# Kernel optimization log

Measured on AMD Instinct MI355X. Metric: run time of the kernel, lower is better.

Reference implementation:

```python
import jax, jax.numpy as jnp
import numpy as np

EPS = 1e-05


def setup_inputs() -> dict:
    key = jax.random.key(0)
    ks = jax.random.split(key, 4)
    B, N, D, H, E = 16, 8192, 128, 64, 64
    x = jax.random.normal(ks[0], (B, N, D), dtype=jnp.float32)
    ln_w = jnp.ones((D,), jnp.float32)
    ln_b = jnp.zeros((D,), jnp.float32)
    Wl = jax.random.normal(ks[1], (D, H), dtype=jnp.float32) / np.sqrt(D)
    bl = jnp.zeros((H,), jnp.float32)
    Wr = jax.random.normal(ks[2], (D, H), dtype=jnp.float32) / np.sqrt(D)
    br = jnp.zeros((H,), jnp.float32)
    Wo = jax.random.normal(ks[3], (H, E), dtype=jnp.float32) / np.sqrt(H)
    bo = jnp.zeros((E,), jnp.float32)
    return {"x": x, "ln_w": ln_w, "ln_b": ln_b, "Wl": Wl, "bl": bl,
            "Wr": Wr, "br": br, "Wo": Wo, "bo": bo}


def _layernorm(x, w, b):
    mu = jnp.mean(x, axis=-1, keepdims=True)
    var = jnp.mean(jnp.square(x - mu), axis=-1, keepdims=True)
    return (x - mu) * jax.lax.rsqrt(var + EPS) * w + b


def reference(x, ln_w, ln_b, Wl, bl, Wr, br, Wo, bo):
    # x: [B, N, D]
    xn = _layernorm(x, ln_w, ln_b)
    left = xn @ Wl + bl    # [B, N, H]
    right = xn @ Wr + br   # [B, N, H]
    # Original: einsum('b i d, b j d -> b i j d').mean(dim=1).
    # Identical math without the O(N^2) tensor: mean over i factors out of
    # the product since left[b,i,d]*right[b,j,d] is separable in i.
    outer = left.mean(axis=1)[:, None, :] * right  # [B, N, H]
    return outer @ Wo + bo  # [B, N, E]
```

## Files before the change

kernel.cpp:

```cpp
#include <hip/hip_runtime.h>
#include <math.h>

#define B_  16
#define N_  8192
#define D_  128
#define H_  64
#define E_  64
#define EPSLN 1e-5f

typedef __attribute__((ext_vector_type(8))) short short8;
typedef __attribute__((ext_vector_type(4))) float f32x4;

#define WSB_COL 0
#define WSB_MT  8192
#define WSB_T   270336
#define WSB_C   274432

static __device__ __forceinline__ unsigned short f2bf(float f) {
    union { float f; unsigned u; } c; c.f = f;
    unsigned u = c.u;
    return (unsigned short)((u + 0x7FFFu + ((u >> 16) & 1u)) >> 16);
}

__global__ __launch_bounds__(256) void k_stats(const float* __restrict__ x,
                                               float* __restrict__ colacc) {
    __shared__ float xs[64 * 132];
    __shared__ float mul[64], rsl[64], red[128];
    int b = blockIdx.y, t = threadIdx.x;
    int rowbase = blockIdx.x * 64;
    size_t gbase = (size_t)(b * N_ + rowbase) * 32;

    const float4* x4 = (const float4*)x;
#pragma unroll
    for (int k = 0; k < 8; ++k) {
        int idx = t + 256 * k;
        int row = idx >> 5, c4 = idx & 31;
        *(float4*)&xs[row * 132 + c4 * 4] = x4[gbase + idx];
    }
    __syncthreads();

    {
        int r = t >> 2, q = t & 3;
        float s = 0.f, s2 = 0.f;
#pragma unroll
        for (int i = 0; i < 8; ++i) {
            float4 v = *(const float4*)&xs[r * 132 + q * 32 + i * 4];
            s  += (v.x + v.y) + (v.z + v.w);
            s2 += (v.x * v.x + v.y * v.y) + (v.z * v.z + v.w * v.w);
        }
        s  += __shfl_xor(s, 1, 64);  s  += __shfl_xor(s, 2, 64);
        s2 += __shfl_xor(s2, 1, 64); s2 += __shfl_xor(s2, 2, 64);
        if (q == 0) {
            float mu  = s * (1.f / D_);
            float var = s2 * (1.f / D_) - mu * mu;
            mul[r] = mu;
            rsl[r] = rsqrtf(var + EPSLN);
        }
    }
    __syncthreads();

    int c = t & 127, hh = t >> 7;
    float acc = 0.f;
#pragma unroll 8
    for (int i = 0; i < 32; ++i) {
        int r = hh * 32 + i;
        acc += rsl[r] * (xs[r * 132 + c] - mul[r]);
    }
    if (hh == 1) red[c] = acc;
    __syncthreads();
    if (hh == 0) atomicAdd(&colacc[b * D_ + c], acc + red[c]);
}

__global__ __launch_bounds__(256) void k_combine(const float* __restrict__ colacc,
                                                 const float* __restrict__ ln_w,
                                                 const float* __restrict__ ln_b,
                                                 const float* __restrict__ Wl,
                                                 const float* __restrict__ bl,
                                                 const float* __restrict__ Wr,
                                                 const float* __restrict__ br,
                                                 const float* __restrict__ Wo,
                                                 const float* __restrict__ bo,
                                                 unsigned short* __restrict__ Mt,
                                                 float* __restrict__ Tg,
                                                 float* __restrict__ Cg) {
    int b = blockIdx.y, dblk = blockIdx.x, t = threadIdx.x;
    __shared__ float cm[D_], ml[H_], uu[H_], qq[H_];
    __shared__ float P[H_ * E_];

    if (t < D_) cm[t] = ln_w[t] * colacc[b * D_ + t] * (1.f / N_) + ln_b[t];
    __syncthreads();

    if (t < H_) {
        float a = bl[t], u = 0.f, q = 0.f;
        for (int d = 0; d < D_; ++d) {
            float wr = Wr[d * H_ + t];
            a += cm[d] * Wl[d * H_ + t];
            u += ln_w[d] * wr;
            q += ln_b[d] * wr;
        }
        ml[t] = a; uu[t] = u; qq[t] = q + br[t];
    }
    __syncthreads();

#pragma unroll
    for (int k = 0; k < 16; ++k) {
        int idx = t + 256 * k;
        P[idx] = ml[idx >> 6] * Wo[idx];
    }
    __syncthreads();

    int d  = dblk * 32 + (t >> 3);
    int eo = (t & 7) * 8;
    float a0 = 0, a1 = 0, a2 = 0, a3 = 0, a4 = 0, a5 = 0, a6 = 0, a7 = 0;
    for (int h = 0; h < H_; ++h) {
        float wr = Wr[d * H_ + h];
        const float4* p4 = (const float4*)&P[h * E_ + eo];
        float4 pa = p4[0], pb = p4[1];
        a0 += wr * pa.x; a1 += wr * pa.y; a2 += wr * pa.z; a3 += wr * pa.w;
        a4 += wr * pb.x; a5 += wr * pb.y; a6 += wr * pb.z; a7 += wr * pb.w;
    }
    float wd = ln_w[d];
    size_t mb = (size_t)b * E_ * D_;
    Mt[mb + (size_t)(eo + 0) * D_ + d] = f2bf(wd * a0);
    Mt[mb + (size_t)(eo + 1) * D_ + d] = f2bf(wd * a1);
    Mt[mb + (size_t)(eo + 2) * D_ + d] = f2bf(wd * a2);
    Mt[mb + (size_t)(eo + 3) * D_ + d] = f2bf(wd * a3);
    Mt[mb + (size_t)(eo + 4) * D_ + d] = f2bf(wd * a4);
    Mt[mb + (size_t)(eo + 5) * D_ + d] = f2bf(wd * a5);
    Mt[mb + (size_t)(eo + 6) * D_ + d] = f2bf(wd * a6);
    Mt[mb + (size_t)(eo + 7) * D_ + d] = f2bf(wd * a7);

    if (dblk == 0 && t < E_) {
        float T = 0.f, C = bo[t];
        for (int h = 0; h < H_; ++h) {
            float p = P[h * E_ + t];
            T += uu[h] * p;
            C += qq[h] * p;
        }
        Tg[b * E_ + t] = T;
        Cg[b * E_ + t] = C;
    }
}

__global__ __launch_bounds__(256, 2) void k_gemm(const float* __restrict__ x,
                                                 const unsigned short* __restrict__ Mt,
                                                 const float* __restrict__ Tg,
                                                 const float* __restrict__ Cg,
                                                 float* __restrict__ out) {
    __shared__ short xs[256 * 128];
    __shared__ float mul[256], rsl[256], Tl[E_], Cl[E_];

    int b = blockIdx.y, t = threadIdx.x;
    int rowbase = blockIdx.x * 256;

    if (t < E_) { Tl[t] = Tg[b * E_ + t]; Cl[t] = Cg[b * E_ + t]; }

    {
        const float4* xrow = (const float4*)(x + (size_t)(b * N_ + rowbase + t) * D_);
        float s = 0.f, s2 = 0.f;
        int sw = t & 15;
#pragma unroll
        for (int g = 0; g < 16; ++g) {
            float4 va = xrow[2 * g], vb = xrow[2 * g + 1];
            s  += (va.x + va.y) + (va.z + va.w) + (vb.x + vb.y) + (vb.z + vb.w);
            s2 += (va.x * va.x + va.y * va.y) + (va.z * va.z + va.w * va.w)
                + (vb.x * vb.x + vb.y * vb.y) + (vb.z * vb.z + vb.w * vb.w);
            short8 sv;
            sv[0] = (short)f2bf(va.x); sv[1] = (short)f2bf(va.y);
            sv[2] = (short)f2bf(va.z); sv[3] = (short)f2bf(va.w);
            sv[4] = (short)f2bf(vb.x); sv[5] = (short)f2bf(vb.y);
            sv[6] = (short)f2bf(vb.z); sv[7] = (short)f2bf(vb.w);
            *(short8*)&xs[t * 128 + ((g ^ sw) * 8)] = sv;
        }
        float mu  = s * (1.f / D_);
        float var = s2 * (1.f / D_) - mu * mu;
        mul[t] = mu;
        rsl[t] = rsqrtf(var + EPSLN);
    }
    __syncthreads();

    int wv = t >> 6, lane = t & 63;
    int m16 = lane & 15, quad = lane >> 4;

    f32x4 acc[4][4];
#pragma unroll
    for (int i = 0; i < 4; ++i)
#pragma unroll
        for (int j = 0; j < 4; ++j) acc[i][j] = (f32x4){0.f, 0.f, 0.f, 0.f};

    const unsigned short* Mb = Mt + (size_t)b * E_ * D_;

#pragma unroll
    for (int kc = 0; kc < 4; ++kc) {
        short8 af[4], bf[4];
#pragma unroll
        for (int mt = 0; mt < 4; ++mt) {
            int row = wv * 64 + mt * 16 + m16;
            int g = kc * 4 + quad;
            af[mt] = *(const short8*)&xs[row * 128 + ((g ^ m16) * 8)];
        }
#pragma unroll
        for (int nt = 0; nt < 4; ++nt) {
            bf[nt] = *(const short8*)(Mb + (size_t)(nt * 16 + m16) * D_ + kc * 32 + quad * 8);
        }
#pragma unroll
        for (int mt = 0; mt < 4; ++mt)
#pragma unroll
            for (int nt = 0; nt < 4; ++nt)
                acc[mt][nt] = __builtin_amdgcn_mfma_f32_16x16x32_bf16(
                    af[mt], bf[nt], acc[mt][nt], 0, 0, 0);
    }

    size_t outbase = (size_t)(b * N_ + rowbase) * E_;
#pragma unroll
    for (int mt = 0; mt < 4; ++mt) {
        int rb = wv * 64 + mt * 16 + quad * 4;
        float mu0 = mul[rb + 0], rs0 = rsl[rb + 0];
        float mu1 = mul[rb + 1], rs1 = rsl[rb + 1];
        float mu2 = mul[rb + 2], rs2 = rsl[rb + 2];
        float mu3 = mul[rb + 3], rs3 = rsl[rb + 3];
#pragma unroll
        for (int nt = 0; nt < 4; ++nt) {
            int col = nt * 16 + m16;
            float Tc = Tl[col], Cc = Cl[col];
            float* o = out + outbase + (size_t)rb * E_ + col;
            o[0 * E_] = rs0 * (acc[mt][nt][0] - mu0 * Tc) + Cc;
            o[1 * E_] = rs1 * (acc[mt][nt][1] - mu1 * Tc) + Cc;
            o[2 * E_] = rs2 * (acc[mt][nt][2] - mu2 * Tc) + Cc;
            o[3 * E_] = rs3 * (acc[mt][nt][3] - mu3 * Tc) + Cc;
        }
    }
}

extern "C" void kernel_launch(void* const* d_in, const int* in_sizes, int n_in,
                              void* d_out, int out_size, void* d_ws, size_t ws_size,
                              hipStream_t stream) {
    const float* x    = (const float*)d_in[0];
    const float* ln_w = (const float*)d_in[1];
    const float* ln_b = (const float*)d_in[2];
    const float* Wl   = (const float*)d_in[3];
    const float* bl   = (const float*)d_in[4];
    const float* Wr   = (const float*)d_in[5];
    const float* br   = (const float*)d_in[6];
    const float* Wo   = (const float*)d_in[7];
    const float* bo   = (const float*)d_in[8];
    float* out = (float*)d_out;
    char* ws   = (char*)d_ws;

    float*          colacc = (float*)(ws + WSB_COL);
    unsigned short* Mt     = (unsigned short*)(ws + WSB_MT);
    float*          Tg     = (float*)(ws + WSB_T);
    float*          Cg     = (float*)(ws + WSB_C);

    hipMemsetAsync(colacc, 0, B_ * D_ * sizeof(float), stream);

    k_stats<<<dim3(N_ / 64, B_), 256, 0, stream>>>(x, colacc);
    k_combine<<<dim3(4, B_), 256, 0, stream>>>(colacc, ln_w, ln_b, Wl, bl, Wr,
                                               br, Wo, bo, Mt, Tg, Cg);
    k_gemm<<<dim3(N_ / 256, B_), 256, 0, stream>>>(x, Mt, Tg, Cg, out);
}
```

Baseline: 145.1 us.

## Reassociate outer-product GEMM to read x once via bf16 right intermediate

Drops the separate stats pass over x. The first GEMM pass now computes right = LN(x)@Wr in bf16, writes it to a workspace buffer, and in the same pass produces per-block column partial sums of normalized x. A small combine kernel then builds the per-batch left-mean-scaled Wo matrix and bias. A second MFMA pass multiplies right by that matrix to form the output. This removes one full 64 MB read of x at the cost of writing and re-reading a 16 MB bf16 intermediate, an extra launch, and column sums taken from bf16-rounded x.

```diff
diff --git a/kernel.cpp b/kernel.cpp
--- a/kernel.cpp
+++ b/kernel.cpp
@@ -11,149 +11,66 @@
 typedef __attribute__((ext_vector_type(8))) short short8;
 typedef __attribute__((ext_vector_type(4))) float f32x4;
 
-#define WSB_COL 0
-#define WSB_MT  8192
-#define WSB_T   270336
-#define WSB_C   274432
+#define WSB_PART 0
+#define WSB_WRT  262144
+#define WSB_U    278528
+#define WSB_Q    278784
+#define WSB_W2T  279040
+#define WSB_C2   410112
+#define WSB_Z    1048576
 
 static __device__ __forceinline__ unsigned short f2bf(float f) {
     union { float f; unsigned u; } c; c.f = f;
     unsigned u = c.u;
     return (unsigned short)((u + 0x7FFFu + ((u >> 16) & 1u)) >> 16);
 }
-
-__global__ __launch_bounds__(256) void k_stats(const float* __restrict__ x,
-                                               float* __restrict__ colacc) {
-    __shared__ float xs[64 * 132];
-    __shared__ float mul[64], rsl[64], red[128];
-    int b = blockIdx.y, t = threadIdx.x;
-    int rowbase = blockIdx.x * 64;
-    size_t gbase = (size_t)(b * N_ + rowbase) * 32;
-
-    const float4* x4 = (const float4*)x;
-#pragma unroll
-    for (int k = 0; k < 8; ++k) {
-        int idx = t + 256 * k;
-        int row = idx >> 5, c4 = idx & 31;
-        *(float4*)&xs[row * 132 + c4 * 4] = x4[gbase + idx];
-    }
-    __syncthreads();
-
-    {
-        int r = t >> 2, q = t & 3;
-        float s = 0.f, s2 = 0.f;
-#pragma unroll
-        for (int i = 0; i < 8; ++i) {
-            float4 v = *(const float4*)&xs[r * 132 + q * 32 + i * 4];
-            s  += (v.x + v.y) + (v.z + v.w);
-            s2 += (v.x * v.x + v.y * v.y) + (v.z * v.z + v.w * v.w);
-        }
-        s  += __shfl_xor(s, 1, 64);  s  += __shfl_xor(s, 2, 64);
-        s2 += __shfl_xor(s2, 1, 64); s2 += __shfl_xor(s2, 2, 64);
-        if (q == 0) {
-            float mu  = s * (1.f / D_);
-            float var = s2 * (1.f / D_) - mu * mu;
-            mul[r] = mu;
-            rsl[r] = rsqrtf(var + EPSLN);
-        }
-    }
-    __syncthreads();
-
-    int c = t & 127, hh = t >> 7;
-    float acc = 0.f;
-#pragma unroll 8
+static __device__ __forceinline__ float bf2f(short v) {
+    union { unsigned u; float f; } c;
+    c.u = ((unsigned)(unsigned short)v) << 16;
+    return c.f;
+}
+
+__global__ __launch_bounds__(256) void k_prep(const float* __restrict__ ln_w,
+                                              const float* __restrict__ ln_b,
+                                              const float* __restrict__ Wr,
+                                              unsigned short* __restrict__ Wrt,
+                                              float* __restrict__ ug,
+                                              float* __restrict__ qg) {
+    __shared__ float ru[4][H_], rq[4][H_];
+    int t = threadIdx.x;
+    int h = t & 63, dq = t >> 6;
+    float u = 0.f, q = 0.f;
     for (int i = 0; i < 32; ++i) {
-        int r = hh * 32 + i;
-        acc += rsl[r] * (xs[r * 132 + c] - mul[r]);
-    }
-    if (hh == 1) red[c] = acc;
-    __syncthreads();
-    if (hh == 0) atomicAdd(&colacc[b * D_ + c], acc + red[c]);
-}
-
-__global__ __launch_bounds__(256) void k_combine(const float* __restrict__ colacc,
-                                                 const float* __restrict__ ln_w,
-                                                 const float* __restrict__ ln_b,
-                                                 const float* __restrict__ Wl,
-                                                 const float* __restrict__ bl,
-                                                 const float* __restrict__ Wr,
-                                                 const float* __restrict__ br,
-                                                 const float* __restrict__ Wo,
-                                                 const float* __restrict__ bo,
-                                                 unsigned short* __restrict__ Mt,
-                                                 float* __restrict__ Tg,
-                                                 float* __restrict__ Cg) {
-    int b = blockIdx.y, dblk = blockIdx.x, t = threadIdx.x;
-    __shared__ float cm[D_], ml[H_], uu[H_], qq[H_];
-    __shared__ float P[H_ * E_];
-
-    if (t < D_) cm[t] = ln_w[t] * colacc[b * D_ + t] * (1.f / N_) + ln_b[t];
-    __syncthreads();
-
+        int d = dq * 32 + i;
+        float wr = Wr[d * H_ + h];
+        float lw = ln_w[d];
+        u += lw * wr;
+        q += ln_b[d] * wr;
+        Wrt[h * D_ + d] = f2bf(lw * wr);
+    }
+    ru[dq][h] = u; rq[dq][h] = q;
+    __syncthreads();
     if (t < H_) {
-        float a = bl[t], u = 0.f, q = 0.f;
-        for (int d = 0; d < D_; ++d) {
-            float wr = Wr[d * H_ + t];
-            a += cm[d] * Wl[d * H_ + t];
-            u += ln_w[d] * wr;
-            q += ln_b[d] * wr;
-        }
-        ml[t] = a; uu[t] = u; qq[t] = q + br[t];
-    }
-    __syncthreads();
-
-#pragma unroll
-    for (int k = 0; k < 16; ++k) {
-        int idx = t + 256 * k;
-        P[idx] = ml[idx >> 6] * Wo[idx];
-    }
-    __syncthreads();
-
-    int d  = dblk * 32 + (t >> 3);
-    int eo = (t & 7) * 8;
-    float a0 = 0, a1 = 0, a2 = 0, a3 = 0, a4 = 0, a5 = 0, a6 = 0, a7 = 0;
-    for (int h = 0; h < H_; ++h) {
-        float wr = Wr[d * H_ + h];
-        const float4* p4 = (const float4*)&P[h * E_ + eo];
-        float4 pa = p4[0], pb = p4[1];
-        a0 += wr * pa.x; a1 += wr * pa.y; a2 += wr * pa.z; a3 += wr * pa.w;
-        a4 += wr * pb.x; a5 += wr * pb.y; a6 += wr * pb.z; a7 += wr * pb.w;
-    }
-    float wd = ln_w[d];
-    size_t mb = (size_t)b * E_ * D_;
-    Mt[mb + (size_t)(eo + 0) * D_ + d] = f2bf(wd * a0);
-    Mt[mb + (size_t)(eo + 1) * D_ + d] = f2bf(wd * a1);
-    Mt[mb + (size_t)(eo + 2) * D_ + d] = f2bf(wd * a2);
-    Mt[mb + (size_t)(eo + 3) * D_ + d] = f2bf(wd * a3);
-    Mt[mb + (size_t)(eo + 4) * D_ + d] = f2bf(wd * a4);
-    Mt[mb + (size_t)(eo + 5) * D_ + d] = f2bf(wd * a5);
-    Mt[mb + (size_t)(eo + 6) * D_ + d] = f2bf(wd * a6);
-    Mt[mb + (size_t)(eo + 7) * D_ + d] = f2bf(wd * a7);
-
-    if (dblk == 0 && t < E_) {
-        float T = 0.f, C = bo[t];
-        for (int h = 0; h < H_; ++h) {
-            float p = P[h * E_ + t];
-            T += uu[h] * p;
-            C += qq[h] * p;
-        }
-        Tg[b * E_ + t] = T;
-        Cg[b * E_ + t] = C;
-    }
-}
-
-__global__ __launch_bounds__(256, 2) void k_gemm(const float* __restrict__ x,
-                                                 const unsigned short* __restrict__ Mt,
-                                                 const float* __restrict__ Tg,
-                                                 const float* __restrict__ Cg,
-                                                 float* __restrict__ out) {
+        ug[t] = ru[0][t] + ru[1][t] + ru[2][t] + ru[3][t];
+        qg[t] = rq[0][t] + rq[1][t] + rq[2][t] + rq[3][t];
+    }
+}
+
+__global__ __launch_bounds__(256, 2) void k_pass1(const float* __restrict__ x,
+                                                  const unsigned short* __restrict__ Wrt,
+                                                  const float* __restrict__ ug,
+                                                  const float* __restrict__ qg,
+                                                  float* __restrict__ partials,
+                                                  unsigned short* __restrict__ Zg) {
     __shared__ short xs[256 * 128];
-    __shared__ float mul[256], rsl[256], Tl[E_], Cl[E_];
-
-    int b = blockIdx.y, t = threadIdx.x;
-    int rowbase = blockIdx.x * 256;
-
-    if (t < E_) { Tl[t] = Tg[b * E_ + t]; Cl[t] = Cg[b * E_ + t]; }
+    __shared__ float mul[256], rsl[256];
+    __shared__ float redc[4][128];
+    __shared__ float ush[H_], qsh[H_];
+
+    int b = blockIdx.y, bx = blockIdx.x, t = threadIdx.x;
+    int rowbase = bx * 256;
+
+    if (t < H_) { ush[t] = ug[t]; qsh[t] = qg[t]; }
 
     {
         const float4* xrow = (const float4*)(x + (size_t)(b * N_ + rowbase + t) * D_);
@@ -179,6 +96,27 @@
     }
     __syncthreads();
 
+    {
+        int cp = (t & 63) * 2, q = t >> 6;
+        int g = cp >> 3, jo = cp & 7;
+        float a0 = 0.f, a1 = 0.f;
+#pragma unroll 8
+        for (int i = 0; i < 64; ++i) {
+            int r = q * 64 + i;
+            short2 v = *(const short2*)&xs[r * 128 + ((g ^ (r & 15)) * 8) + jo];
+            float w = rsl[r], m = mul[r];
+            a0 += w * (bf2f(v.x) - m);
+            a1 += w * (bf2f(v.y) - m);
+        }
+        redc[q][cp] = a0;
+        redc[q][cp + 1] = a1;
+    }
+    __syncthreads();
+    if (t < 128) {
+        float s = redc[0][t] + redc[1][t] + redc[2][t] + redc[3][t];
+        partials[(size_t)(b * 32 + bx) * D_ + t] = s;
+    }
+
     int wv = t >> 6, lane = t & 63;
     int m16 = lane & 15, quad = lane >> 4;
 
@@ -187,8 +125,6 @@
     for (int i = 0; i < 4; ++i)
 #pragma unroll
         for (int j = 0; j < 4; ++j) acc[i][j] = (f32x4){0.f, 0.f, 0.f, 0.f};
-
-    const unsigned short* Mb = Mt + (size_t)b * E_ * D_;
 
 #pragma unroll
     for (int kc = 0; kc < 4; ++kc) {
@@ -201,7 +137,7 @@
         }
 #pragma unroll
         for (int nt = 0; nt < 4; ++nt) {
-            bf[nt] = *(const short8*)(Mb + (size_t)(nt * 16 + m16) * D_ + kc * 32 + quad * 8);
+            bf[nt] = *(const short8*)(Wrt + (size_t)(nt * 16 + m16) * D_ + kc * 32 + quad * 8);
         }
 #pragma unroll
         for (int mt = 0; mt < 4; ++mt)
@@ -211,7 +147,7 @@
                     af[mt], bf[nt], acc[mt][nt], 0, 0, 0);
     }
 
-    size_t outbase = (size_t)(b * N_ + rowbase) * E_;
+    size_t zbase = (size_t)(b * N_ + rowbase) * H_;
 #pragma unroll
     for (int mt = 0; mt < 4; ++mt) {
         int rb = wv * 64 + mt * 16 + quad * 4;
@@ -222,12 +158,116 @@
 #pragma unroll
         for (int nt = 0; nt < 4; ++nt) {
             int col = nt * 16 + m16;
-            float Tc = Tl[col], Cc = Cl[col];
+            float uc = ush[col], qc = qsh[col];
+            unsigned short* zp = Zg + zbase + (size_t)rb * H_ + col;
+            zp[0 * H_] = f2bf(rs0 * (acc[mt][nt][0] - mu0 * uc) + qc);
+            zp[1 * H_] = f2bf(rs1 * (acc[mt][nt][1] - mu1 * uc) + qc);
+            zp[2 * H_] = f2bf(rs2 * (acc[mt][nt][2] - mu2 * uc) + qc);
+            zp[3 * H_] = f2bf(rs3 * (acc[mt][nt][3] - mu3 * uc) + qc);
+        }
+    }
+}
+
+__global__ __launch_bounds__(256) void k_combine2(const float* __restrict__ partials,
+                                                  const float* __restrict__ ln_w,
+                                                  const float* __restrict__ ln_b,
+                                                  const float* __restrict__ Wl,
+                                                  const float* __restrict__ bl,
+                                                  const float* __restrict__ br,
+                                                  const float* __restrict__ Wo,
+                                                  const float* __restrict__ bo,
+                                                  unsigned short* __restrict__ W2t,
+                                                  float* __restrict__ C2g) {
+    __shared__ float cm[D_], mlh[H_];
+    __shared__ float redC[4][E_];
+    int b = blockIdx.x, t = threadIdx.x;
+
+    if (t < D_) {
+        float s = 0.f;
+#pragma unroll 8
+        for (int k = 0; k < 32; ++k)
+            s += partials[(size_t)(b * 32 + k) * D_ + t];
+        cm[t] = ln_w[t] * s * (1.f / N_) + ln_b[t];
+    }
+    __syncthreads();
+    if (t < H_) {
+        float a = bl[t];
+        for (int d = 0; d < D_; ++d) a += cm[d] * Wl[d * H_ + t];
+        mlh[t] = a;
+    }
+    __syncthreads();
+
+    int e = t & 63, hq = t >> 6;
+    float cpart = 0.f;
+    size_t wb = (size_t)b * E_ * H_;
+    for (int i = 0; i < 16; ++i) {
+        int h = hq * 16 + i;
+        float wo = Wo[h * E_ + e];
+        float w2 = mlh[h] * wo;
+        cpart += w2 * br[h];
+        W2t[wb + (size_t)e * H_ + h] = f2bf(w2);
+    }
+    redC[hq][e] = cpart;
+    __syncthreads();
+    if (t < E_)
+        C2g[b * E_ + t] = redC[0][t] + redC[1][t] + redC[2][t] + redC[3][t] + bo[t];
+}
+
+__global__ __launch_bounds__(256) void k_pass2(const unsigned short* __restrict__ Zg,
+                                               const unsigned short* __restrict__ W2t,
+                                               const float* __restrict__ C2g,
+                                               float* __restrict__ out) {
+    __shared__ float C2l[E_];
+    int b = blockIdx.y, bx = blockIdx.x, t = threadIdx.x;
+    int rowbase = bx * 256;
+    if (t < E_) C2l[t] = C2g[b * E_ + t];
+    __syncthreads();
+
+    int wv = t >> 6, lane = t & 63;
+    int m16 = lane & 15, quad = lane >> 4;
+
+    f32x4 acc[4][4];
+#pragma unroll
+    for (int i = 0; i < 4; ++i)
+#pragma unroll
+        for (int j = 0; j < 4; ++j) acc[i][j] = (f32x4){0.f, 0.f, 0.f, 0.f};
+
+    size_t zbase = (size_t)(b * N_ + rowbase) * H_;
+    const unsigned short* Wb = W2t + (size_t)b * E_ * H_;
+
+#pragma unroll
+    for (int kc = 0; kc < 2; ++kc) {
+        short8 af[4], bf[4];
+#pragma unroll
+        for (int mt = 0; mt < 4; ++mt) {
+            int row = wv * 64 + mt * 16 + m16;
+            af[mt] = *(const short8*)(Zg + zbase + (size_t)row * H_ + kc * 32 + quad * 8);
+        }
+#pragma unroll
+        for (int nt = 0; nt < 4; ++nt) {
+            bf[nt] = *(const short8*)(Wb + (size_t)(nt * 16 + m16) * H_ + kc * 32 + quad * 8);
+        }
+#pragma unroll
+        for (int mt = 0; mt < 4; ++mt)
+#pragma unroll
+            for (int nt = 0; nt < 4; ++nt)
+                acc[mt][nt] = __builtin_amdgcn_mfma_f32_16x16x32_bf16(
+                    af[mt], bf[nt], acc[mt][nt], 0, 0, 0);
+    }
+
+    size_t outbase = (size_t)(b * N_ + rowbase) * E_;
+#pragma unroll
+    for (int mt = 0; mt < 4; ++mt) {
+        int rb = wv * 64 + mt * 16 + quad * 4;
+#pragma unroll
+        for (int nt = 0; nt < 4; ++nt) {
+            int col = nt * 16 + m16;
+            float Cc = C2l[col];
             float* o = out + outbase + (size_t)rb * E_ + col;
-            o[0 * E_] = rs0 * (acc[mt][nt][0] - mu0 * Tc) + Cc;
-            o[1 * E_] = rs1 * (acc[mt][nt][1] - mu1 * Tc) + Cc;
-            o[2 * E_] = rs2 * (acc[mt][nt][2] - mu2 * Tc) + Cc;
-            o[3 * E_] = rs3 * (acc[mt][nt][3] - mu3 * Tc) + Cc;
+            o[0 * E_] = acc[mt][nt][0] + Cc;
+            o[1 * E_] = acc[mt][nt][1] + Cc;
+            o[2 * E_] = acc[mt][nt][2] + Cc;
+            o[3 * E_] = acc[mt][nt][3] + Cc;
         }
     }
 }
@@ -247,15 +287,17 @@
     float* out = (float*)d_out;
     char* ws   = (char*)d_ws;
 
-    float*          colacc = (float*)(ws + WSB_COL);
-    unsigned short* Mt     = (unsigned short*)(ws + WSB_MT);
-    float*          Tg     = (float*)(ws + WSB_T);
-    float*          Cg     = (float*)(ws + WSB_C);
-
-    hipMemsetAsync(colacc, 0, B_ * D_ * sizeof(float), stream);
-
-    k_stats<<<dim3(N_ / 64, B_), 256, 0, stream>>>(x, colacc);
-    k_combine<<<dim3(4, B_), 256, 0, stream>>>(colacc, ln_w, ln_b, Wl, bl, Wr,
-                                               br, Wo, bo, Mt, Tg, Cg);
-    k_gemm<<<dim3(N_ / 256, B_), 256, 0, stream>>>(x, Mt, Tg, Cg, out);
-}
+    float*          partials = (float*)(ws + WSB_PART);
+    unsigned short* Wrt      = (unsigned short*)(ws + WSB_WRT);
+    float*          ug       = (float*)(ws + WSB_U);
+    float*          qg       = (float*)(ws + WSB_Q);
+    unsigned short* W2t      = (unsigned short*)(ws + WSB_W2T);
+    float*          C2g      = (float*)(ws + WSB_C2);
+    unsigned short* Zg       = (unsigned short*)(ws + WSB_Z);
+
+    k_prep<<<1, 256, 0, stream>>>(ln_w, ln_b, Wr, Wrt, ug, qg);
+    k_pass1<<<dim3(32, B_), 256, 0, stream>>>(x, Wrt, ug, qg, partials, Zg);
+    k_combine2<<<B_, 256, 0, stream>>>(partials, ln_w, ln_b, Wl, bl, br, Wo,
+                                       bo, W2t, C2g);
+    k_pass2<<<dim3(32, B_), 256, 0, stream>>>(Zg, W2t, C2g, out);
+}
```

Result: slower. 148.8 us (+2.5%).
